# Kernel tuning notes

Hardware: AMD Instinct MI355X
Metric: run time of the kernel (lower is better)

## Reference

```python
import jax, jax.numpy as jnp
import numpy as np

N_NODES = 100000
N_EDGES = 640000
IN_CH = 128
OUT_CH = 128


def setup_inputs() -> dict:
    key = jax.random.key(0)
    k1, k2, k3, k4, k5, k6 = jax.random.split(key, 6)
    row = jax.random.randint(k1, (N_EDGES,), 0, N_NODES, dtype=jnp.int64 if jax.config.jax_enable_x64 else jnp.int32)
    col = jax.random.randint(k2, (N_EDGES,), 0, N_NODES, dtype=jnp.int64 if jax.config.jax_enable_x64 else jnp.int32)
    vals = jax.random.uniform(k3, (N_EDGES,), dtype=jnp.float32)
    X = jax.random.normal(k4, (N_NODES, IN_CH), dtype=jnp.float32)
    weights = jax.random.normal(k5, (IN_CH, OUT_CH), dtype=jnp.float32)
    bias = jax.random.normal(k6, (OUT_CH,), dtype=jnp.float32)
    return {"row": row, "col": col, "vals": vals, "X": X, "weights": weights, "bias": bias}


def reference(row, col, vals, X, weights, bias):
    # A is sparse COO: A[row[e], col[e]] = vals[e]
    N = X.shape[0]
    # dense feature transform: [N, out]
    XTheta = X @ weights
    # D = (row_sum(A) + 1)^(-1/2)
    deg = jax.ops.segment_sum(vals, row, num_segments=N)
    D = jax.lax.rsqrt(deg + 1.0)
    # Xprime = D * (A @ (D * XTheta))
    Y = D[:, None] * XTheta                                    # [N, out]
    msgs = vals[:, None] * Y[col]                              # [E, out] gather
    AY = jax.ops.segment_sum(msgs, row, num_segments=N)        # [N, out] scatter-add
    return D[:, None] * AY + bias
```

## Files before the change

### kernel.cpp

```cpp
#include <hip/hip_runtime.h>
#include <hip/hip_bf16.h>


#define N_CH 128
#define WT_LD 136
#define FIXS 16777216.0f
#define KMAX 64

typedef __attribute__((ext_vector_type(8))) short short8;
typedef __attribute__((ext_vector_type(4))) float f32x4;
typedef __attribute__((ext_vector_type(4))) unsigned short ushort4v;

__device__ inline unsigned short f2bf(float f) {
    unsigned u = __float_as_uint(f);
    return (unsigned short)((u + 0x7FFFu + ((u >> 16) & 1u)) >> 16);
}
__device__ inline float bf2f(unsigned short h) {
    return __uint_as_float(((unsigned)h) << 16);
}

__global__ __launch_bounds__(256) void init_kernel(const float* __restrict__ W,
                                                   unsigned short* __restrict__ Wt,
                                                   unsigned long long* __restrict__ packed,
                                                   int N) {
    int gid = blockIdx.x * 256 + threadIdx.x;
    for (int i = gid; i < N; i += (int)gridDim.x * 256) packed[i] = 0ULL;
    if (gid < N_CH * N_CH) {
        int n = gid >> 7, k = gid & 127;
        Wt[n * N_CH + k] = f2bf(W[k * N_CH + n]);
    }
}

__global__ __launch_bounds__(256) void build_gemm_kernel(
        const int* __restrict__ row, const int* __restrict__ col,
        const float* __restrict__ vals, const float* __restrict__ X,
        const unsigned short* __restrict__ Wt,
        unsigned long long* __restrict__ packed, uint2* __restrict__ epack,
        unsigned short* __restrict__ Ybf, int N, int E, int gemmBlocks) {
    __shared__ unsigned short Wl[N_CH * WT_LD];

    const int t = threadIdx.x;

    if ((int)blockIdx.x >= gemmBlocks) {
        int e0 = (blockIdx.x - gemmBlocks) * 512 + t;
#pragma unroll
        for (int j = 0; j < 2; ++j) {
            int e = e0 + j * 256;
            if (e < E) {
                int r = row[e];
                float v = vals[e];
                unsigned fx = (unsigned)(v * FIXS);
                unsigned long long old =
                    atomicAdd(&packed[r], (1ULL << 32) | (unsigned long long)fx);
                unsigned slot = (unsigned)(old >> 32);
                if (slot < KMAX)
                    epack[(size_t)r * KMAX + slot] =
                        make_uint2((unsigned)col[e], __float_as_uint(v));
            }
        }
        return;
    }

    const short8* Wg = (const short8*)Wt;
#pragma unroll
    for (int j = 0; j < 8; ++j) {
        int idx = t + 256 * j;
        int r = idx >> 4, cc = idx & 15;
        *(short8*)(Wl + r * WT_LD + cc * 8) = Wg[idx];
    }
    __syncthreads();

    const int lane = t & 63;
    const int wv = t >> 6;
    const int m = lane & 15;
    const int q = lane >> 4;

    const int tiles = (N + 15) / 16;
    const int totalWaves = gemmBlocks * 4;
    int tile = blockIdx.x * 4 + wv;
    if (tile >= tiles) return;

    f32x4 pl[4], ph[4];
    {
        int rr = tile * 16 + m;
        if (rr >= N) rr = N - 1;
        const float* xr = X + (size_t)rr * N_CH + q * 8;
#pragma unroll
        for (int c = 0; c < 4; ++c) {
            pl[c] = *(const f32x4*)(xr + c * 32);
            ph[c] = *(const f32x4*)(xr + c * 32 + 4);
        }
    }

    while (true) {
        const int next = tile + totalWaves;
        const bool hasNext = next < tiles;

        f32x4 ql[4], qh[4];
        if (hasNext) {
            int rr2 = next * 16 + m;
            if (rr2 >= N) rr2 = N - 1;
            const float* xr2 = X + (size_t)rr2 * N_CH + q * 8;
#pragma unroll
            for (int c = 0; c < 4; ++c) {
                ql[c] = *(const f32x4*)(xr2 + c * 32);
                qh[c] = *(const f32x4*)(xr2 + c * 32 + 4);
            }
        }

        short8 a[4];
#pragma unroll
        for (int c = 0; c < 4; ++c) {
            short8 v;
            v[0] = (short)f2bf(pl[c][0]); v[1] = (short)f2bf(pl[c][1]);
            v[2] = (short)f2bf(pl[c][2]); v[3] = (short)f2bf(pl[c][3]);
            v[4] = (short)f2bf(ph[c][0]); v[5] = (short)f2bf(ph[c][1]);
            v[6] = (short)f2bf(ph[c][2]); v[7] = (short)f2bf(ph[c][3]);
            a[c] = v;
        }

        f32x4 acc[8];
#pragma unroll
        for (int tt = 0; tt < 8; ++tt) acc[tt] = (f32x4){0.f, 0.f, 0.f, 0.f};

#pragma unroll
        for (int tt = 0; tt < 8; ++tt) {
            const unsigned short* wrow = Wl + (tt * 16 + m) * WT_LD + q * 8;
#pragma unroll
            for (int c = 0; c < 4; ++c) {
                short8 b = *(const short8*)(wrow + c * 32);
                acc[tt] = __builtin_amdgcn_mfma_f32_16x16x32_bf16(b, a[c], acc[tt], 0, 0, 0);
            }
        }

        const int rr = tile * 16 + m;
        if (rr < N) {
            unsigned short* yrow = Ybf + (size_t)rr * N_CH;
#pragma unroll
            for (int tt = 0; tt < 8; ++tt) {
                unsigned lo = (unsigned)f2bf(acc[tt][0]) |
                              ((unsigned)f2bf(acc[tt][1]) << 16);
                unsigned hi = (unsigned)f2bf(acc[tt][2]) |
                              ((unsigned)f2bf(acc[tt][3]) << 16);
                *(uint2*)(yrow + tt * 16 + q * 4) = make_uint2(lo, hi);
            }
        }

        if (!hasNext) break;
#pragma unroll
        for (int c = 0; c < 4; ++c) { pl[c] = ql[c]; ph[c] = qh[c]; }
        tile = next;
    }
}

__global__ __launch_bounds__(256) void gather_kernel(
        const unsigned long long* __restrict__ packed,
        const uint2* __restrict__ epack,
        const unsigned short* __restrict__ Ybf,
        const float* __restrict__ bias,
        float* __restrict__ out, int N) {
    unsigned gid = blockIdx.x * 256u + threadIdx.x;
    int n = gid >> 5;
    if (n >= N) return;
    int lane = gid & 31;
    int c = lane * 4;

    unsigned long long pk = packed[n];
    int cnt = (int)(pk >> 32);
    if (cnt > KMAX) cnt = KMAX;
    float dn = rsqrtf((float)(unsigned)(pk & 0xFFFFFFFFull) * (1.0f / FIXS) + 1.0f);
    const uint2* base = epack + (size_t)n * KMAX;

    float4 acc = make_float4(0.f, 0.f, 0.f, 0.f);
    int e = 0;
    for (; e + 4 <= cnt; e += 4) {
        uint2 p0 = base[e + 0];
        uint2 p1 = base[e + 1];
        uint2 p2 = base[e + 2];
        uint2 p3 = base[e + 3];
        unsigned long long k0 = packed[p0.x];
        unsigned long long k1 = packed[p1.x];
        unsigned long long k2 = packed[p2.x];
        unsigned long long k3 = packed[p3.x];
        ushort4v y0 = *(const ushort4v*)(Ybf + (size_t)p0.x * N_CH + c);
        ushort4v y1 = *(const ushort4v*)(Ybf + (size_t)p1.x * N_CH + c);
        ushort4v y2 = *(const ushort4v*)(Ybf + (size_t)p2.x * N_CH + c);
        ushort4v y3 = *(const ushort4v*)(Ybf + (size_t)p3.x * N_CH + c);
        float w0 = __uint_as_float(p0.y) *
                   rsqrtf((float)(unsigned)(k0 & 0xFFFFFFFFull) * (1.0f / FIXS) + 1.0f);
        float w1 = __uint_as_float(p1.y) *
                   rsqrtf((float)(unsigned)(k1 & 0xFFFFFFFFull) * (1.0f / FIXS) + 1.0f);
        float w2 = __uint_as_float(p2.y) *
                   rsqrtf((float)(unsigned)(k2 & 0xFFFFFFFFull) * (1.0f / FIXS) + 1.0f);
        float w3 = __uint_as_float(p3.y) *
                   rsqrtf((float)(unsigned)(k3 & 0xFFFFFFFFull) * (1.0f / FIXS) + 1.0f);
        acc.x += w0 * bf2f(y0[0]) + w1 * bf2f(y1[0]) + w2 * bf2f(y2[0]) + w3 * bf2f(y3[0]);
        acc.y += w0 * bf2f(y0[1]) + w1 * bf2f(y1[1]) + w2 * bf2f(y2[1]) + w3 * bf2f(y3[1]);
        acc.z += w0 * bf2f(y0[2]) + w1 * bf2f(y1[2]) + w2 * bf2f(y2[2]) + w3 * bf2f(y3[2]);
        acc.w += w0 * bf2f(y0[3]) + w1 * bf2f(y1[3]) + w2 * bf2f(y2[3]) + w3 * bf2f(y3[3]);
    }
    for (; e < cnt; ++e) {
        uint2 p = base[e];
        unsigned long long kk = packed[p.x];
        float w = __uint_as_float(p.y) *
                  rsqrtf((float)(unsigned)(kk & 0xFFFFFFFFull) * (1.0f / FIXS) + 1.0f);
        ushort4v y = *(const ushort4v*)(Ybf + (size_t)p.x * N_CH + c);
        acc.x += w * bf2f(y[0]);
        acc.y += w * bf2f(y[1]);
        acc.z += w * bf2f(y[2]);
        acc.w += w * bf2f(y[3]);
    }

    float4 b = ((const float4*)bias)[lane];
    float4 o;
    o.x = acc.x * dn + b.x;
    o.y = acc.y * dn + b.y;
    o.z = acc.z * dn + b.z;
    o.w = acc.w * dn + b.w;
    ((float4*)(out + (size_t)n * N_CH))[lane] = o;
}

extern "C" void kernel_launch(void* const* d_in, const int* in_sizes, int n_in,
                              void* d_out, int out_size, void* d_ws, size_t ws_size,
                              hipStream_t stream) {
    const int*   row  = (const int*)d_in[0];
    const int*   col  = (const int*)d_in[1];
    const float* vals = (const float*)d_in[2];
    const float* X    = (const float*)d_in[3];
    const float* W    = (const float*)d_in[4];
    const float* bias = (const float*)d_in[5];
    float* out = (float*)d_out;

    const int E = in_sizes[0];
    const int N = in_sizes[3] / N_CH;

    uint2*              epack  = (uint2*)d_ws;
    unsigned short*     Ybf    = (unsigned short*)(epack + (size_t)N * KMAX);
    unsigned long long* packed = (unsigned long long*)(Ybf + (size_t)N * N_CH);
    unsigned short*     Wt     = (unsigned short*)(packed + N);

    init_kernel<<<512, 256, 0, stream>>>(W, Wt, packed, N);

    const int gemmBlocks = 512;
    const int buildBlocks = (E + 511) / 512;
    build_gemm_kernel<<<gemmBlocks + buildBlocks, 256, 0, stream>>>(
        row, col, vals, X, Wt, packed, epack, Ybf, N, E, gemmBlocks);

    unsigned gth = (unsigned)N * 32u;
    gather_kernel<<<(gth + 255) / 256, 256, 0, stream>>>(packed, epack, Ybf,
                                                         bias, out, N);
}
```

Baseline: 189.6 us.

## Inline row header into edge records and precompute inverse-sqrt degrees

Each node's counter/degree word now sits at the head of its 64-entry edge record, so the atomic and the gather's header read share a cache line with the first edges. A new small kernel precomputes the inverse-sqrt degree into a compact float array, so the gather does 4-byte dinv lookups instead of 8-byte packed loads followed by an rsqrt per neighbor. The first four edge entries are loaded before the count is known, to cut dependent latency. The cost is an extra kernel launch and one fewer slot per row (63 instead of 64).

```diff
diff --git a/kernel.cpp b/kernel.cpp
--- a/kernel.cpp
+++ b/kernel.cpp
@@ -5,7 +5,7 @@
 #define N_CH 128
 #define WT_LD 136
 #define FIXS 16777216.0f
-#define KMAX 64
+#define KSLOT 63
 
 typedef __attribute__((ext_vector_type(8))) short short8;
 typedef __attribute__((ext_vector_type(4))) float f32x4;
@@ -21,10 +21,11 @@
 
 __global__ __launch_bounds__(256) void init_kernel(const float* __restrict__ W,
                                                    unsigned short* __restrict__ Wt,
-                                                   unsigned long long* __restrict__ packed,
+                                                   uint2* __restrict__ erec,
                                                    int N) {
     int gid = blockIdx.x * 256 + threadIdx.x;
-    for (int i = gid; i < N; i += (int)gridDim.x * 256) packed[i] = 0ULL;
+    for (int i = gid; i < N; i += (int)gridDim.x * 256)
+        *(unsigned long long*)(erec + (size_t)i * 64) = 0ULL;
     if (gid < N_CH * N_CH) {
         int n = gid >> 7, k = gid & 127;
         Wt[n * N_CH + k] = f2bf(W[k * N_CH + n]);
@@ -35,8 +36,8 @@
         const int* __restrict__ row, const int* __restrict__ col,
         const float* __restrict__ vals, const float* __restrict__ X,
         const unsigned short* __restrict__ Wt,
-        unsigned long long* __restrict__ packed, uint2* __restrict__ epack,
-        unsigned short* __restrict__ Ybf, int N, int E, int gemmBlocks) {
+        uint2* __restrict__ erec, unsigned short* __restrict__ Ybf,
+        int N, int E, int gemmBlocks) {
     __shared__ unsigned short Wl[N_CH * WT_LD];
 
     const int t = threadIdx.x;
@@ -50,11 +51,12 @@
                 int r = row[e];
                 float v = vals[e];
                 unsigned fx = (unsigned)(v * FIXS);
-                unsigned long long old =
-                    atomicAdd(&packed[r], (1ULL << 32) | (unsigned long long)fx);
+                unsigned long long old = atomicAdd(
+                    (unsigned long long*)(erec + (size_t)r * 64),
+                    (1ULL << 32) | (unsigned long long)fx);
                 unsigned slot = (unsigned)(old >> 32);
-                if (slot < KMAX)
-                    epack[(size_t)r * KMAX + slot] =
+                if (slot < KSLOT)
+                    erec[(size_t)r * 64 + 1 + slot] =
                         make_uint2((unsigned)col[e], __float_as_uint(v));
             }
         }
@@ -153,10 +155,19 @@
     }
 }
 
+__global__ __launch_bounds__(256) void dinv_kernel(const uint2* __restrict__ erec,
+                                                   float* __restrict__ dinv, int N) {
+    int n = blockIdx.x * 256 + threadIdx.x;
+    if (n < N) {
+        unsigned long long h = *(const unsigned long long*)(erec + (size_t)n * 64);
+        dinv[n] = rsqrtf((float)(unsigned)(h & 0xFFFFFFFFull) * (1.0f / FIXS) + 1.0f);
+    }
+}
+
 __global__ __launch_bounds__(256) void gather_kernel(
-        const unsigned long long* __restrict__ packed,
-        const uint2* __restrict__ epack,
+        const uint2* __restrict__ erec,
         const unsigned short* __restrict__ Ybf,
+        const float* __restrict__ dinv,
         const float* __restrict__ bias,
         float* __restrict__ out, int N) {
     unsigned gid = blockIdx.x * 256u + threadIdx.x;
@@ -165,45 +176,54 @@
     int lane = gid & 31;
     int c = lane * 4;
 
-    unsigned long long pk = packed[n];
+    const uint2* base = erec + (size_t)n * 64;
+    uint2 f0 = base[1];
+    uint2 f1 = base[2];
+    uint2 f2 = base[3];
+    uint2 f3 = base[4];
+    unsigned long long pk = *(const unsigned long long*)base;
     int cnt = (int)(pk >> 32);
-    if (cnt > KMAX) cnt = KMAX;
-    float dn = rsqrtf((float)(unsigned)(pk & 0xFFFFFFFFull) * (1.0f / FIXS) + 1.0f);
-    const uint2* base = epack + (size_t)n * KMAX;
+    if (cnt > KSLOT) cnt = KSLOT;
+    float dn = dinv[n];
 
     float4 acc = make_float4(0.f, 0.f, 0.f, 0.f);
     int e = 0;
-    for (; e + 4 <= cnt; e += 4) {
-        uint2 p0 = base[e + 0];
-        uint2 p1 = base[e + 1];
-        uint2 p2 = base[e + 2];
-        uint2 p3 = base[e + 3];
-        unsigned long long k0 = packed[p0.x];
-        unsigned long long k1 = packed[p1.x];
-        unsigned long long k2 = packed[p2.x];
-        unsigned long long k3 = packed[p3.x];
-        ushort4v y0 = *(const ushort4v*)(Ybf + (size_t)p0.x * N_CH + c);
-        ushort4v y1 = *(const ushort4v*)(Ybf + (size_t)p1.x * N_CH + c);
-        ushort4v y2 = *(const ushort4v*)(Ybf + (size_t)p2.x * N_CH + c);
-        ushort4v y3 = *(const ushort4v*)(Ybf + (size_t)p3.x * N_CH + c);
-        float w0 = __uint_as_float(p0.y) *
-                   rsqrtf((float)(unsigned)(k0 & 0xFFFFFFFFull) * (1.0f / FIXS) + 1.0f);
-        float w1 = __uint_as_float(p1.y) *
-                   rsqrtf((float)(unsigned)(k1 & 0xFFFFFFFFull) * (1.0f / FIXS) + 1.0f);
-        float w2 = __uint_as_float(p2.y) *
-                   rsqrtf((float)(unsigned)(k2 & 0xFFFFFFFFull) * (1.0f / FIXS) + 1.0f);
-        float w3 = __uint_as_float(p3.y) *
-                   rsqrtf((float)(unsigned)(k3 & 0xFFFFFFFFull) * (1.0f / FIXS) + 1.0f);
+    if (cnt >= 4) {
+        float w0 = __uint_as_float(f0.y) * dinv[f0.x];
+        float w1 = __uint_as_float(f1.y) * dinv[f1.x];
+        float w2 = __uint_as_float(f2.y) * dinv[f2.x];
+        float w3 = __uint_as_float(f3.y) * dinv[f3.x];
+        ushort4v y0 = *(const ushort4v*)(Ybf + (size_t)f0.x * N_CH + c);
+        ushort4v y1 = *(const ushort4v*)(Ybf + (size_t)f1.x * N_CH + c);
+        ushort4v y2 = *(const ushort4v*)(Ybf + (size_t)f2.x * N_CH + c);
+        ushort4v y3 = *(const ushort4v*)(Ybf + (size_t)f3.x * N_CH + c);
         acc.x += w0 * bf2f(y0[0]) + w1 * bf2f(y1[0]) + w2 * bf2f(y2[0]) + w3 * bf2f(y3[0]);
         acc.y += w0 * bf2f(y0[1]) + w1 * bf2f(y1[1]) + w2 * bf2f(y2[1]) + w3 * bf2f(y3[1]);
         acc.z += w0 * bf2f(y0[2]) + w1 * bf2f(y1[2]) + w2 * bf2f(y2[2]) + w3 * bf2f(y3[2]);
         acc.w += w0 * bf2f(y0[3]) + w1 * bf2f(y1[3]) + w2 * bf2f(y2[3]) + w3 * bf2f(y3[3]);
+        e = 4;
+        for (; e + 4 <= cnt; e += 4) {
+            uint2 p0 = base[1 + e + 0];
+            uint2 p1 = base[1 + e + 1];
+            uint2 p2 = base[1 + e + 2];
+            uint2 p3 = base[1 + e + 3];
+            float v0 = __uint_as_float(p0.y) * dinv[p0.x];
+            float v1 = __uint_as_float(p1.y) * dinv[p1.x];
+            float v2 = __uint_as_float(p2.y) * dinv[p2.x];
+            float v3 = __uint_as_float(p3.y) * dinv[p3.x];
+            ushort4v z0 = *(const ushort4v*)(Ybf + (size_t)p0.x * N_CH + c);
+            ushort4v z1 = *(const ushort4v*)(Ybf + (size_t)p1.x * N_CH + c);
+            ushort4v z2 = *(const ushort4v*)(Ybf + (size_t)p2.x * N_CH + c);
+            ushort4v z3 = *(const ushort4v*)(Ybf + (size_t)p3.x * N_CH + c);
+            acc.x += v0 * bf2f(z0[0]) + v1 * bf2f(z1[0]) + v2 * bf2f(z2[0]) + v3 * bf2f(z3[0]);
+            acc.y += v0 * bf2f(z0[1]) + v1 * bf2f(z1[1]) + v2 * bf2f(z2[1]) + v3 * bf2f(z3[1]);
+            acc.z += v0 * bf2f(z0[2]) + v1 * bf2f(z1[2]) + v2 * bf2f(z2[2]) + v3 * bf2f(z3[2]);
+            acc.w += v0 * bf2f(z0[3]) + v1 * bf2f(z1[3]) + v2 * bf2f(z2[3]) + v3 * bf2f(z3[3]);
+        }
     }
     for (; e < cnt; ++e) {
-        uint2 p = base[e];
-        unsigned long long kk = packed[p.x];
-        float w = __uint_as_float(p.y) *
-                  rsqrtf((float)(unsigned)(kk & 0xFFFFFFFFull) * (1.0f / FIXS) + 1.0f);
+        uint2 p = base[1 + e];
+        float w = __uint_as_float(p.y) * dinv[p.x];
         ushort4v y = *(const ushort4v*)(Ybf + (size_t)p.x * N_CH + c);
         acc.x += w * bf2f(y[0]);
         acc.y += w * bf2f(y[1]);
@@ -234,19 +254,21 @@
     const int E = in_sizes[0];
     const int N = in_sizes[3] / N_CH;
 
-    uint2*              epack  = (uint2*)d_ws;
-    unsigned short*     Ybf    = (unsigned short*)(epack + (size_t)N * KMAX);
-    unsigned long long* packed = (unsigned long long*)(Ybf + (size_t)N * N_CH);
-    unsigned short*     Wt     = (unsigned short*)(packed + N);
-
-    init_kernel<<<512, 256, 0, stream>>>(W, Wt, packed, N);
+    uint2*          erec = (uint2*)d_ws;
+    unsigned short* Ybf  = (unsigned short*)(erec + (size_t)N * 64);
+    float*          dinv = (float*)(Ybf + (size_t)N * N_CH);
+    unsigned short* Wt   = (unsigned short*)(dinv + N);
+
+    init_kernel<<<512, 256, 0, stream>>>(W, Wt, erec, N);
 
     const int gemmBlocks = 512;
     const int buildBlocks = (E + 511) / 512;
     build_gemm_kernel<<<gemmBlocks + buildBlocks, 256, 0, stream>>>(
-        row, col, vals, X, Wt, packed, epack, Ybf, N, E, gemmBlocks);
+        row, col, vals, X, Wt, erec, Ybf, N, E, gemmBlocks);
+
+    dinv_kernel<<<(N + 255) / 256, 256, 0, stream>>>(erec, dinv, N);
 
     unsigned gth = (unsigned)N * 32u;
-    gather_kernel<<<(gth + 255) / 256, 256, 0, stream>>>(packed, epack, Ybf,
+    gather_kernel<<<(gth + 255) / 256, 256, 0, stream>>>(erec, Ybf, dinv,
                                                          bias, out, N);
 }
```

Result: slower. 198.5 us (+4.7%).
